# Kernel tuning notes

Measured on AMD Instinct MI355X. Metric: run time of the kernel, lower is better.

## Reference

```python
import jax, jax.numpy as jnp
import numpy as np

D_MODEL = 64      # init_kwargs d_model
MAX_RANGE = 1.0   # init_kwargs max_range
N_POINTS = 1_000_000


def _positional_encoding(n):
    # encoding[i, 2j]   = sin(i / 10000**(2j/d_model))
    # encoding[i, 2j+1] = cos(i / 10000**(2j/d_model))
    i = jnp.arange(n, dtype=jnp.float32)[:, None]                 # [N, 1]
    j = jnp.arange(D_MODEL // 2, dtype=jnp.float32)[None, :]      # [1, D/2]
    pos_val = i / jnp.power(jnp.float32(10000.0), 2.0 * j / D_MODEL)  # [N, D/2]
    enc = jnp.stack([jnp.sin(pos_val), jnp.cos(pos_val)], axis=-1)    # [N, D/2, 2]
    enc = enc.reshape(n, 2 * (D_MODEL // 2))
    if 2 * (D_MODEL // 2) < D_MODEL:  # odd d_model: last column stays zero
        enc = jnp.pad(enc, ((0, 0), (0, D_MODEL - 2 * (D_MODEL // 2))))
    return MAX_RANGE * enc


def setup_inputs() -> dict:
    key = jax.random.key(0)
    point_cloud = jax.random.normal(key, (N_POINTS, 6), dtype=jnp.float32)
    return {"point_cloud": point_cloud}


def reference(point_cloud):
    n = point_cloud.shape[0]
    coords = point_cloud[:, :3]
    colours = point_cloud[:, 3:]
    enc = _positional_encoding(n)
    return jnp.concatenate([coords, enc, colours], axis=1)  # [N, 6 + d_model]
```

## Files before the change

### kernel.cpp

```cpp
#include <hip/hip_runtime.h>
#include <math.h>


#define OUTC 70

__global__ __launch_bounds__(256) void pe_kernel(const float* __restrict__ pc,
                                                 float* __restrict__ out,
                                                 long long total) {
    __shared__ double s_invfreq[32];
    const int tid = threadIdx.x;
    if (tid < 32) {
        s_invfreq[tid] = exp(-(double)tid * (log(10000.0) / 32.0));
    }
    __syncthreads();

    const long long base = ((long long)blockIdx.x * blockDim.x + tid) * 4;
    if (base >= total) return;

    const double two_pi     = 6.283185307179586476925286766559;
    const double inv_two_pi = 0.15915494309189533576888376337251;

    float4 v;
    float* ve = &v.x;

#pragma unroll
    for (int k = 0; k < 4; ++k) {
        const long long idx = base + k;
        const int row = (int)(idx / OUTC);
        const int col = (int)(idx - (long long)row * OUTC);
        float r;
        if (col < 3) {
            r = pc[row * 6 + col];
        } else if (col >= 67) {
            r = pc[row * 6 + (col - 64)];
        } else {
            const int e = col - 3;
            const int j = e >> 1;
            const double arg = (double)row * s_invfreq[j];
            const double kk  = rint(arg * inv_two_pi);
            const double red = fma(-kk, two_pi, arg);
            const float rf = (float)red;
            float s, c;
            __sincosf(rf, &s, &c);
            r = (e & 1) ? c : s;
        }
        ve[k] = r;
    }

    const long long last = base + 3;
    if (last < total) {
        reinterpret_cast<float4*>(out)[base >> 2] = v;
    } else {
        for (int k = 0; k < 4; ++k)
            if (base + k < total) out[base + k] = ve[k];
    }
}

extern "C" void kernel_launch(void* const* d_in, const int* in_sizes, int n_in,
                              void* d_out, int out_size, void* d_ws, size_t ws_size,
                              hipStream_t stream) {
    const float* pc = (const float*)d_in[0];
    float* out = (float*)d_out;
    const long long n = in_sizes[0] / 6;
    const long long total = n * OUTC;
    const long long n_threads = (total + 3) / 4;
    const int block = 256;
    const long long grid = (n_threads + block - 1) / block;
    pe_kernel<<<dim3((unsigned)grid), dim3(block), 0, stream>>>(pc, out, total);
}
```

Measured before the change: 330.0 us.

## Stage row tiles in shared memory and compute one sincos per frequency pair

The kernel is restructured so each block owns 32 full rows. The block computes the sin/cos pair for each (row, frequency) once into a shared-memory tile, loads the input coordinates and colours with float4 reads scattered into the tile, then writes the tile out with coalesced float4 stores. This removes the per-element divide by 70, the divergent branches, and the duplicate sincos work where neighbouring output elements shared one argument. Range reduction now uses a prescaled frequency and a fractional part. The cost is extra shared memory, a second barrier, and possible bank conflicts from the stride-70 tile layout.

```diff
diff --git a/kernel.cpp b/kernel.cpp
--- a/kernel.cpp
+++ b/kernel.cpp
@@ -2,57 +2,89 @@
 #include <math.h>
 
 
+#define ROWS_PER_BLOCK 32
 #define OUTC 70
+#define FLOATS_PER_BLOCK (ROWS_PER_BLOCK * OUTC)
+#define VEC4_PER_BLOCK   (FLOATS_PER_BLOCK / 4)
+#define IN_FLOATS_PER_BLOCK (ROWS_PER_BLOCK * 6)
+#define IN_VEC4_PER_BLOCK   (IN_FLOATS_PER_BLOCK/4)
 
 __global__ __launch_bounds__(256) void pe_kernel(const float* __restrict__ pc,
                                                  float* __restrict__ out,
-                                                 long long total) {
-    __shared__ double s_invfreq[32];
+                                                 int n_rows) {
+    __shared__ float  s_tile[FLOATS_PER_BLOCK];
+    __shared__ double s_w2[32];
+
     const int tid = threadIdx.x;
+    const int b = blockIdx.x;
+    const int rowBase = b * ROWS_PER_BLOCK;
+
     if (tid < 32) {
-        s_invfreq[tid] = exp(-(double)tid * (log(10000.0) / 32.0));
+        s_w2[tid] = 0.15915494309189533577 * exp(-(double)tid * (log(10000.0) / 32.0));
     }
     __syncthreads();
 
-    const long long base = ((long long)blockIdx.x * blockDim.x + tid) * 4;
-    if (base >= total) return;
-
-    const double two_pi     = 6.283185307179586476925286766559;
-    const double inv_two_pi = 0.15915494309189533576888376337251;
-
-    float4 v;
-    float* ve = &v.x;
-
+    const int j = tid & 31;
+    const double w2 = s_w2[j];
+    const double two_pi = 6.2831853071795864769;
+    int r = tid >> 5;
 #pragma unroll
     for (int k = 0; k < 4; ++k) {
-        const long long idx = base + k;
-        const int row = (int)(idx / OUTC);
-        const int col = (int)(idx - (long long)row * OUTC);
-        float r;
-        if (col < 3) {
-            r = pc[row * 6 + col];
-        } else if (col >= 67) {
-            r = pc[row * 6 + (col - 64)];
-        } else {
-            const int e = col - 3;
-            const int j = e >> 1;
-            const double arg = (double)row * s_invfreq[j];
-            const double kk  = rint(arg * inv_two_pi);
-            const double red = fma(-kk, two_pi, arg);
-            const float rf = (float)red;
-            float s, c;
-            __sincosf(rf, &s, &c);
-            r = (e & 1) ? c : s;
-        }
-        ve[k] = r;
+        const double t = (double)(rowBase + r) * w2;
+        const double frac = t - rint(t);
+        const float rad = (float)(frac * two_pi);
+        const int pos = r * OUTC + 3 + 2 * j;
+        s_tile[pos]     = __sinf(rad);
+        s_tile[pos + 1] = __cosf(rad);
+        r += 8;
     }
 
-    const long long last = base + 3;
-    if (last < total) {
-        reinterpret_cast<float4*>(out)[base >> 2] = v;
-    } else {
-        for (int k = 0; k < 4; ++k)
-            if (base + k < total) out[base + k] = ve[k];
+    if (tid < IN_VEC4_PER_BLOCK) {
+        const long long inBase = (long long)b * IN_FLOATS_PER_BLOCK;
+        const long long f0 = inBase + tid * 4;
+        const long long in_total = (long long)n_rows * 6;
+        if (f0 + 3 < in_total) {
+            const float4 v = reinterpret_cast<const float4*>(pc)[inBase / 4 + tid];
+            const float* ve = &v.x;
+#pragma unroll
+            for (int m = 0; m < 4; ++m) {
+                const int fl = tid * 4 + m;
+                const int row = fl / 6;
+                const int c = fl - row * 6;
+                const int col = (c < 3) ? c : (c + 64);
+                s_tile[row * OUTC + col] = ve[m];
+            }
+        } else {
+            for (int m = 0; m < 4; ++m) {
+                const long long f = f0 + m;
+                if (f < in_total) {
+                    const float val = pc[f];
+                    const int fl = tid * 4 + m;
+                    const int row = fl / 6;
+                    const int c = fl - row * 6;
+                    const int col = (c < 3) ? c : (c + 64);
+                    s_tile[row * OUTC + col] = val;
+                }
+            }
+        }
+    }
+    __syncthreads();
+
+    const long long outBase = (long long)b * FLOATS_PER_BLOCK;
+    const long long total = (long long)n_rows * OUTC;
+    for (int i = tid; i < VEC4_PER_BLOCK; i += 256) {
+        const long long g = outBase + (long long)i * 4;
+        if (g + 4 <= total) {
+            float4 v;
+            v.x = s_tile[i * 4 + 0];
+            v.y = s_tile[i * 4 + 1];
+            v.z = s_tile[i * 4 + 2];
+            v.w = s_tile[i * 4 + 3];
+            reinterpret_cast<float4*>(out)[outBase / 4 + i] = v;
+        } else {
+            for (int m = 0; m < 4; ++m)
+                if (g + m < total) out[g + m] = s_tile[i * 4 + m];
+        }
     }
 }
 
@@ -61,10 +93,7 @@
                               hipStream_t stream) {
     const float* pc = (const float*)d_in[0];
     float* out = (float*)d_out;
-    const long long n = in_sizes[0] / 6;
-    const long long total = n * OUTC;
-    const long long n_threads = (total + 3) / 4;
-    const int block = 256;
-    const long long grid = (n_threads + block - 1) / block;
-    pe_kernel<<<dim3((unsigned)grid), dim3(block), 0, stream>>>(pc, out, total);
+    const int n_rows = in_sizes[0] / 6;
+    const int grid = (n_rows + ROWS_PER_BLOCK - 1) / ROWS_PER_BLOCK;
+    pe_kernel<<<dim3(grid), dim3(256), 0, stream>>>(pc, out, n_rows);
 }
```

New measurement: 292.7 us. 11.3% less time.
